# Optimization experiments

Measured on AMD Instinct MI355X. Metric: run time of the kernel, lower is better.

Reference implementation:

```python
import jax, jax.numpy as jnp
import numpy as np

B, N, E = 16, 2048, 1_048_576          # graphs, residues per graph, total edges
IN_C, DIM, OUT_C, ENC_H, N_ATOMS = 256, 128, 6, 100, 20
NT = B * N


def setup_inputs() -> dict:
    key = jax.random.key(0)
    ks = jax.random.split(key, 24)
    s = 0.02
    x_res = jax.random.normal(ks[0], (NT, IN_C), jnp.float32)
    coords = jax.random.normal(ks[1], (NT, 3), jnp.float32)
    batch = jnp.repeat(jnp.arange(B, dtype=jnp.int32), N)
    src = jax.random.randint(ks[2], (E,), 0, NT, dtype=jnp.int32)
    dst = (src // N) * N + jax.random.randint(ks[3], (E,), 0, N, dtype=jnp.int32)
    edge_index = jnp.stack([src, dst])  # intra-graph edges, global node ids
    return {
        'x_res': x_res, 'coords': coords,
        'edge_index': edge_index, 'batch': batch,
        'bn_gamma': jnp.ones((IN_C,), jnp.float32),
        'bn_beta': jnp.zeros((IN_C,), jnp.float32),
        'W1': s * jax.random.normal(ks[4], (IN_C, 2 * DIM), jnp.float32),
        'b1': jnp.zeros((2 * DIM,), jnp.float32),
        'W2': s * jax.random.normal(ks[5], (2 * DIM, DIM), jnp.float32),
        'b2': jnp.zeros((DIM,), jnp.float32),
        'W3': s * jax.random.normal(ks[6], (DIM, N_ATOMS), jnp.float32),
        'b3': jnp.zeros((N_ATOMS,), jnp.float32),
        'embed': s * jax.random.normal(ks[7], (N_ATOMS + 1, DIM), jnp.float32),
        'W_msg': s * jax.random.normal(ks[8], (DIM, DIM), jnp.float32),
        'b_msg': jnp.zeros((DIM,), jnp.float32),
        'w_coor': s * jax.random.normal(ks[9], (DIM, 3), jnp.float32),
        'A1': s * jax.random.normal(ks[10], (DIM, ENC_H), jnp.float32),
        'a1': jnp.zeros((ENC_H,), jnp.float32),
        'A2': s * jax.random.normal(ks[11], (ENC_H, OUT_C), jnp.float32),
        'a2': jnp.zeros((OUT_C,), jnp.float32),
        'dyt_alpha': jnp.float32(0.5),
        'dyt_w': jnp.ones((OUT_C,), jnp.float32),
        'dyt_b': jnp.zeros((OUT_C,), jnp.float32),
    }


def reference(x_res, coords, edge_index, batch,
              bn_gamma, bn_beta, W1, b1, W2, b2, W3, b3,
              embed, W_msg, b_msg, w_coor,
              A1, a1, A2, a2, dyt_alpha, dyt_w, dyt_b):
    gelu = lambda v: jax.nn.gelu(v, approximate=False)
    # BatchNorm1d (train-mode batch stats, biased var, eps=1e-5); dropout is identity in eval
    mu = x_res.mean(0)
    var = x_res.var(0)
    xn = (x_res - mu) / jnp.sqrt(var + 1e-5) * bn_gamma + bn_beta
    # input2atomids MLP -> argmax atom ids
    h1 = gelu(xn @ W1 + b1)
    h2 = gelu(h1 @ W2 + b2)
    logits = h2 @ W3 + b3
    ids = jnp.argmax(logits, axis=-1)          # [NT]
    ids_b = ids.reshape(B, N)                  # equal-sized graphs -> no padding needed
    coords_b = coords.reshape(B, N, 3)
    # vectorized edge-list -> dense per-graph adjacency scatter
    g = batch[edge_index[0]]                   # graph id per edge
    ls = edge_index[0] - g * N                 # local src index
    ld = edge_index[1] - g * N                 # local dst index
    same = batch[edge_index[1]] == g           # keep intra-graph edges only
    adj = jnp.zeros((B, N, N), jnp.bool_).at[g, ls, ld].max(same)
    # GotenNet stand-in: embed atom ids, one adjacency-masked aggregation layer
    emb_ids = jnp.where(ids_b < 0, N_ATOMS, ids_b)   # -1 pad -> pad embedding row
    h = embed[emb_ids]                          # [B,N,DIM]
    adjf = adj.astype(h.dtype)
    deg = jnp.maximum(adjf.sum(-1, keepdims=True), 1.0)
    m = jnp.einsum('bij,bjd->bid', adjf, h) / deg
    hout = gelu((h + m) @ W_msg + b_msg)        # invariant features [B,N,DIM]
    coors_out = coords_b + jnp.tanh(hout @ w_coor)
    # un-pad / flatten back to node list, then out_angles head
    z = hout.reshape(NT, DIM)
    t = gelu(z @ A1 + a1)
    t = gelu(t @ A2 + a2)
    t = jnp.tanh(dyt_alpha * t) * dyt_w + dyt_b  # DynamicTanh (channels_last)
    angles = jnp.tanh(t)                         # [NT, OUT_C]
    return angles, z, coors_out
```

## Files before the change

kernel.cpp:

```cpp
#include <hip/hip_runtime.h>
#include <hip/hip_bf16.h>
#include <math.h>

#define Bg 16
#define Nn 2048
#define Ee (1<<20)
#define NT (Bg*Nn)
#define INC 256
#define DIMd 128
#define OUTC 6
#define ENCH 100
#define NATOMS 20
#define BINCAP 3072

typedef __attribute__((ext_vector_type(8))) short bf16x8;
typedef __attribute__((ext_vector_type(4))) float f32x4;

__device__ __forceinline__ float gelu_f(float x){
    return 0.5f*x*(1.0f+erff(x*0.70710678118654752440f));
}
__device__ __forceinline__ unsigned short f2b(float f){
    __hip_bfloat16 h = __float2bfloat16(f);
    return *(unsigned short*)&h;
}
__device__ __forceinline__ float b2f(unsigned short u){
    unsigned v = ((unsigned)u)<<16;
    return __uint_as_float(v);
}
__device__ __forceinline__ void splitf(float v, unsigned short& hi, unsigned short& lo){
    unsigned short h = f2b(v);
    hi = h; lo = f2b(v - b2f(h));
}

__global__ __launch_bounds__(256) void prep0_k(const float* __restrict__ x,
    float* __restrict__ stats, const float* __restrict__ W1,
    const float* __restrict__ W2, const float* __restrict__ Wm,
    const float* __restrict__ A1, short* __restrict__ w1th, short* __restrict__ w1tl,
    short* __restrict__ w2th, short* __restrict__ w2tl,
    short* __restrict__ wmth, short* __restrict__ wmtl,
    short* __restrict__ a1th, short* __restrict__ a1tl)
{
    int bx = blockIdx.x, tid = threadIdx.x;
    if(bx < 256){
        int c = tid;
        int r0 = bx * 128;
        const float* p = x + (size_t)r0*INC + c;
        float s = 0.f, s2 = 0.f;
        #pragma unroll 8
        for(int r=0;r<128;r++){ float v = p[(size_t)r*INC]; s += v; s2 += v*v; }
        atomicAdd(&stats[c], s);
        atomicAdd(&stats[INC+c], s2);
    } else {
        int gid = (bx-256)*256 + tid;
        unsigned short hi, lo;
        for(int l=gid;l<65536;l+=16384){ int n=l>>8,k=l&255;
            splitf(W1[(size_t)k*256+n],hi,lo); w1th[l]=(short)hi; w1tl[l]=(short)lo; }
        for(int l=gid;l<32768;l+=16384){ int n=l>>8,k=l&255;
            splitf(W2[(size_t)k*128+n],hi,lo); w2th[l]=(short)hi; w2tl[l]=(short)lo; }
        for(int l=gid;l<16384;l+=16384){ int n=l>>7,k=l&127;
            splitf(Wm[(size_t)k*128+n],hi,lo); wmth[l]=(short)hi; wmtl[l]=(short)lo; }
        for(int l=gid;l<16384;l+=16384){ int n=l>>7,k=l&127;
            float v=(n<ENCH)? A1[(size_t)k*ENCH+n] : 0.f;
            splitf(v,hi,lo); a1th[l]=(short)hi; a1tl[l]=(short)lo; }
    }
}

__global__ __launch_bounds__(256) void gemm1_scat_k(const float* __restrict__ x,
    const float* __restrict__ stats, const float* __restrict__ gamma,
    const float* __restrict__ beta, const short* __restrict__ w1th,
    const short* __restrict__ w1tl, const float* __restrict__ b1,
    unsigned short* __restrict__ h1h, unsigned short* __restrict__ h1l,
    const int* __restrict__ ei, unsigned* __restrict__ ecnt,
    unsigned* __restrict__ earena)
{
    __shared__ float sc[256], sh[256];
    __shared__ short sAh[64*40], sAl[64*40];
    __shared__ short sBh[256*40], sBl[256*40];
    int tid = threadIdx.x;
    {
        float mu  = stats[tid]*(1.0f/NT);
        float var = stats[256+tid]*(1.0f/NT) - mu*mu;
        float s = gamma[tid]/sqrtf(var + 1e-5f);
        sc[tid] = s; sh[tid] = beta[tid] - mu*s;
    }
    int row0 = blockIdx.x*64;
    int lane = tid&63, w = tid>>6;
    int ln = lane&15, quad = lane>>4;
    int m0w = (w&1)*32, n0b = (w>>1)*128;
    f32x4 acc[2][8];
    #pragma unroll
    for(int i=0;i<2;i++)
        #pragma unroll
        for(int j=0;j<8;j++) acc[i][j] = (f32x4){0.f,0.f,0.f,0.f};

    float4 xa[2]; bf16x8 wb[8];
    #pragma unroll
    for(int i=0;i<2;i++){ int id=tid+i*256; int r=id>>3,kq=(id&7)*4;
        xa[i] = *(const float4*)&x[(size_t)(row0+r)*256 + kq]; }
    #pragma unroll
    for(int i=0;i<8;i++){ int id=tid+i*256; int plane=id>>10,cid=id&1023;
        int r=cid>>2,c=cid&3;
        wb[i] = *(const bf16x8*)((plane? w1tl:w1th) + (size_t)r*256 + c*8); }
    __syncthreads();
    for(int k0=0;k0<256;k0+=32){
        #pragma unroll
        for(int i=0;i<2;i++){
            int id = tid + i*256; int r = id>>3, kq = (id&7)*4;
            int k = k0+kq;
            float v0 = xa[i].x*sc[k]+sh[k],   v1 = xa[i].y*sc[k+1]+sh[k+1];
            float v2 = xa[i].z*sc[k+2]+sh[k+2], v3 = xa[i].w*sc[k+3]+sh[k+3];
            ushort4 hi, lo;
            splitf(v0,hi.x,lo.x); splitf(v1,hi.y,lo.y);
            splitf(v2,hi.z,lo.z); splitf(v3,hi.w,lo.w);
            *(ushort4*)&sAh[r*40+kq] = hi;
            *(ushort4*)&sAl[r*40+kq] = lo;
        }
        #pragma unroll
        for(int i=0;i<8;i++){
            int id = tid + i*256; int plane = id>>10, cid = id&1023;
            int r = cid>>2, c = cid&3;
            *(bf16x8*)((plane? sBl : sBh) + r*40 + c*8) = wb[i];
        }
        __syncthreads();
        if(k0 < 224){
            #pragma unroll
            for(int i=0;i<2;i++){ int id=tid+i*256; int r=id>>3,kq=(id&7)*4;
                xa[i] = *(const float4*)&x[(size_t)(row0+r)*256 + k0+32+kq]; }
            #pragma unroll
            for(int i=0;i<8;i++){ int id=tid+i*256; int plane=id>>10,cid=id&1023;
                int r=cid>>2,c=cid&3;
                wb[i] = *(const bf16x8*)((plane? w1tl:w1th) + (size_t)r*256 + k0+32 + c*8); }
        }
        bf16x8 ah[2], al[2];
        #pragma unroll
        for(int tm=0;tm<2;tm++){
            ah[tm] = *(const bf16x8*)&sAh[(m0w+tm*16+ln)*40 + quad*8];
            al[tm] = *(const bf16x8*)&sAl[(m0w+tm*16+ln)*40 + quad*8];
        }
        #pragma unroll
        for(int tn=0;tn<8;tn++){
            bf16x8 bh = *(const bf16x8*)&sBh[(n0b+tn*16+ln)*40 + quad*8];
            bf16x8 bl = *(const bf16x8*)&sBl[(n0b+tn*16+ln)*40 + quad*8];
            #pragma unroll
            for(int tm=0;tm<2;tm++){
                acc[tm][tn] = __builtin_amdgcn_mfma_f32_16x16x32_bf16(al[tm], bh, acc[tm][tn], 0,0,0);
                acc[tm][tn] = __builtin_amdgcn_mfma_f32_16x16x32_bf16(ah[tm], bl, acc[tm][tn], 0,0,0);
                acc[tm][tn] = __builtin_amdgcn_mfma_f32_16x16x32_bf16(ah[tm], bh, acc[tm][tn], 0,0,0);
            }
        }
        __syncthreads();
    }
    #pragma unroll
    for(int tn=0;tn<8;tn++){
        int col = n0b + tn*16 + ln;
        float bias = b1[col];
        #pragma unroll
        for(int tm=0;tm<2;tm++){
            int rowb = row0 + m0w + tm*16 + quad*4;
            #pragma unroll
            for(int r=0;r<4;r++){
                float hv = gelu_f(acc[tm][tn][r] + bias);
                unsigned short hi, lo;
                splitf(hv, hi, lo);
                h1h[(size_t)(rowb+r)*256 + col] = hi;
                h1l[(size_t)(rowb+r)*256 + col] = lo;
            }
        }
    }
    if(blockIdx.x < 128){
        __syncthreads();
        unsigned* lcnt  = (unsigned*)sAh;
        unsigned* gbase = ((unsigned*)sAh) + 512;
        for(int l=tid; l<512; l+=256) lcnt[l] = 0;
        __syncthreads();
        int ebase = blockIdx.x * 8192;
        #pragma unroll 8
        for(int i=0;i<32;i++){
            int e = ebase + i*256 + tid;
            int s = ei[e], d = ei[Ee+e];
            if((s>>11)==(d>>11)) atomicAdd(&lcnt[s>>6], 1u);
        }
        __syncthreads();
        for(int l=tid; l<512; l+=256){
            unsigned c = lcnt[l];
            gbase[l] = c ? atomicAdd(&ecnt[l], c) : 0u;
            lcnt[l] = 0;
        }
        __syncthreads();
        #pragma unroll 8
        for(int i=0;i<32;i++){
            int e = ebase + i*256 + tid;
            int s = ei[e], d = ei[Ee+e];
            if((s>>11)==(d>>11)){
                int bin = s>>6;
                unsigned r = atomicAdd(&lcnt[bin], 1u);
                unsigned pos = gbase[bin] + r;
                if(pos < BINCAP)
                    earena[(size_t)bin*BINCAP + pos] =
                        ((unsigned)(s&63)<<11) | (unsigned)(d&2047);
            }
        }
    }
}

__global__ __launch_bounds__(256) void gemm23_mfma(
    const unsigned short* __restrict__ h1h, const unsigned short* __restrict__ h1l,
    const short* __restrict__ w2th, const short* __restrict__ w2tl,
    const float* __restrict__ b2, const float* __restrict__ W3,
    const float* __restrict__ b3, int* __restrict__ ids)
{
    __shared__ short sAh[64*40], sAl[64*40];
    __shared__ short sBh[128*40], sBl[128*40];
    __shared__ float h2s[64*132];
    __shared__ float lgs[64*20];
    int tid = threadIdx.x;
    int row0 = blockIdx.x*64;
    int lane = tid&63, w = tid>>6;
    int ln = lane&15, quad = lane>>4;
    int m0w = (w&1)*32, n0w = (w>>1)*64;
    f32x4 acc[2][4];
    #pragma unroll
    for(int i=0;i<2;i++)
        #pragma unroll
        for(int j=0;j<4;j++) acc[i][j] = (f32x4){0.f,0.f,0.f,0.f};

    bf16x8 ha[2], wb[4];
    #pragma unroll
    for(int i=0;i<2;i++){ int id=tid+i*256; int plane=id>>8,cid=id&255;
        int r=cid>>2,c=cid&3;
        ha[i] = *(const bf16x8*)((const short*)(plane? h1l : h1h)
                                 + (size_t)(row0+r)*256 + c*8); }
    #pragma unroll
    for(int i=0;i<4;i++){ int id=tid+i*256; int plane=id>>9,cid=id&511;
        int r=cid>>2,c=cid&3;
        wb[i] = *(const bf16x8*)((plane? w2tl:w2th) + (size_t)r*256 + c*8); }
    for(int k0=0;k0<256;k0+=32){
        #pragma unroll
        for(int i=0;i<2;i++){
            int id = tid + i*256; int plane = id>>8, cid = id&255;
            int r = cid>>2, c = cid&3;
            *(bf16x8*)((plane? sAl : sAh) + r*40 + c*8) = ha[i];
        }
        #pragma unroll
        for(int i=0;i<4;i++){
            int id = tid + i*256; int plane = id>>9, cid = id&511;
            int r = cid>>2, c = cid&3;
            *(bf16x8*)((plane? sBl : sBh) + r*40 + c*8) = wb[i];
        }
        __syncthreads();
        if(k0 < 224){
            #pragma unroll
            for(int i=0;i<2;i++){ int id=tid+i*256; int plane=id>>8,cid=id&255;
                int r=cid>>2,c=cid&3;
                ha[i] = *(const bf16x8*)((const short*)(plane? h1l : h1h)
                                         + (size_t)(row0+r)*256 + k0+32 + c*8); }
            #pragma unroll
            for(int i=0;i<4;i++){ int id=tid+i*256; int plane=id>>9,cid=id&511;
                int r=cid>>2,c=cid&3;
                wb[i] = *(const bf16x8*)((plane? w2tl:w2th) + (size_t)r*256 + k0+32 + c*8); }
        }
        bf16x8 ah[2], al[2];
        #pragma unroll
        for(int tm=0;tm<2;tm++){
            ah[tm] = *(const bf16x8*)&sAh[(m0w+tm*16+ln)*40 + quad*8];
            al[tm] = *(const bf16x8*)&sAl[(m0w+tm*16+ln)*40 + quad*8];
        }
        #pragma unroll
        for(int tn=0;tn<4;tn++){
            bf16x8 bh = *(const bf16x8*)&sBh[(n0w+tn*16+ln)*40 + quad*8];
            bf16x8 bl = *(const bf16x8*)&sBl[(n0w+tn*16+ln)*40 + quad*8];
            #pragma unroll
            for(int tm=0;tm<2;tm++){
                acc[tm][tn] = __builtin_amdgcn_mfma_f32_16x16x32_bf16(al[tm], bh, acc[tm][tn], 0,0,0);
                acc[tm][tn] = __builtin_amdgcn_mfma_f32_16x16x32_bf16(ah[tm], bl, acc[tm][tn], 0,0,0);
                acc[tm][tn] = __builtin_amdgcn_mfma_f32_16x16x32_bf16(ah[tm], bh, acc[tm][tn], 0,0,0);
            }
        }
        __syncthreads();
    }
    #pragma unroll
    for(int tn=0;tn<4;tn++){
        int col = n0w + tn*16 + ln;
        float bias = b2[col];
        #pragma unroll
        for(int tm=0;tm<2;tm++){
            int rb = m0w + tm*16 + quad*4;
            #pragma unroll
            for(int r=0;r<4;r++)
                h2s[(rb+r)*132 + col] = gelu_f(acc[tm][tn][r] + bias);
        }
    }
    float* w3s = (float*)sBh;
    for(int l=tid;l<2560;l+=256) w3s[l] = W3[l];
    __syncthreads();
    int n = tid>>2, q = tid&3;
    float lg[5] = {};
    #pragma unroll 4
    for(int k=0;k<128;k++){
        float h = h2s[n*132+k];
        #pragma unroll
        for(int a=0;a<5;a++) lg[a] += h*w3s[k*20 + q*5 + a];
    }
    #pragma unroll
    for(int a=0;a<5;a++) lgs[n*20 + q*5 + a] = lg[a] + b3[q*5+a];
    __syncthreads();
    if(tid<64){
        float best = lgs[tid*20]; int bi = 0;
        #pragma unroll
        for(int a=1;a<20;a++){ float v2 = lgs[tid*20+a]; if(v2>best){best=v2;bi=a;} }
        ids[row0+tid] = bi;
    }
}

__global__ __launch_bounds__(256) void msgA_k(
    const int* __restrict__ ids, const unsigned* __restrict__ ecnt,
    const unsigned* __restrict__ earena, const float* __restrict__ embed,
    unsigned short* __restrict__ vbf)
{
    __shared__ unsigned lmask[64*64];
    __shared__ unsigned ind[NATOMS*64];
    __shared__ unsigned char sid[2048];
    __shared__ float emb[NATOMS*128];
    int tid = threadIdx.x;
    int bin = blockIdx.x;
    int row0 = bin*64;
    int g = bin>>5, tile = bin&31;
    int lane = tid&63, w = tid>>6;

    for(int l=tid;l<NATOMS*128;l+=256) emb[l] = embed[l];
    #pragma unroll
    for(int i=0;i<8;i++){ int j = tid + i*256; sid[j] = (unsigned char)ids[g*Nn + j]; }
    #pragma unroll
    for(int i=0;i<16;i++) lmask[tid + i*256] = 0;
    int nb = min((int)ecnt[bin], BINCAP);
    __syncthreads();

    for(int wp=w; wp<32; wp+=4){
        int a = sid[wp*64 + lane];
        #pragma unroll
        for(int atom=0; atom<NATOMS; atom++){
            unsigned long long bm = __ballot(a==atom);
            if(lane<2) ind[atom*64 + wp*2 + lane] = (unsigned)(bm >> (32*lane));
        }
    }
    for(int i=tid; i<nb; i+=256){
        unsigned wv = earena[(size_t)bin*BINCAP + i];
        int sl = wv>>11, dl = wv & 2047;
        atomicOr(&lmask[sl*64 + (dl>>5)], 1u<<(dl&31));
    }
    __syncthreads();

    int node = tid>>2, p = tid&3;
    unsigned mw[16];
    {
        const unsigned* mrow = &lmask[node*64 + p*16];
        *(uint4*)&mw[0]  = *(const uint4*)&mrow[0];
        *(uint4*)&mw[4]  = *(const uint4*)&mrow[4];
        *(uint4*)&mw[8]  = *(const uint4*)&mrow[8];
        *(uint4*)&mw[12] = *(const uint4*)&mrow[12];
    }
    int degi = 0;
    #pragma unroll
    for(int w2=0;w2<16;w2++) degi += __popc(mw[w2]);
    float cnt[NATOMS];
    #pragma unroll
    for(int a=0;a<NATOMS;a++){
        int c = 0;
        const unsigned* ia = &ind[a*64 + p*16];
        #pragma unroll
        for(int w2=0;w2<16;w2++) c += __popc(mw[w2] & ia[w2]);
        cnt[a] = (float)c;
    }
    #pragma unroll
    for(int a=0;a<NATOMS;a++){
        cnt[a] += __shfl_xor(cnt[a],1,64);
        cnt[a] += __shfl_xor(cnt[a],2,64);
    }
    float deg = (float)degi;
    deg += __shfl_xor(deg,1,64);
    deg += __shfl_xor(deg,2,64);

    {
        float inv = 1.0f / fmaxf(deg, 1.0f);
        int oid = sid[tile*64 + node];
        int d0 = p*32;
        float vv[32];
        #pragma unroll
        for(int d=0;d<32;d++) vv[d]=0.f;
        #pragma unroll
        for(int a=0;a<NATOMS;a++){
            float ca = cnt[a];
            const float* ea = &emb[a*128 + d0];
            #pragma unroll
            for(int d=0;d<32;d+=4){
                float4 e = *(const float4*)&ea[d];
                vv[d]+=ca*e.x; vv[d+1]+=ca*e.y; vv[d+2]+=ca*e.z; vv[d+3]+=ca*e.w;
            }
        }
        const float* eo = &emb[oid*128 + d0];
        unsigned short* dst = vbf + (size_t)(row0+node)*128 + d0;
        #pragma unroll
        for(int d=0;d<32;d+=4){
            float4 e = *(const float4*)&eo[d];
            ushort4 o;
            o.x = f2b(e.x + vv[d]*inv);
            o.y = f2b(e.y + vv[d+1]*inv);
            o.z = f2b(e.z + vv[d+2]*inv);
            o.w = f2b(e.w + vv[d+3]*inv);
            *(ushort4*)&dst[d] = o;
        }
    }
}

__global__ __launch_bounds__(256,4) void msgB_k(
    const unsigned short* __restrict__ vbf,
    const short* __restrict__ wmth, const short* __restrict__ wmtl,
    const float* __restrict__ b_msg, const float* __restrict__ w_coor,
    const short* __restrict__ a1th, const short* __restrict__ a1tl,
    const float* __restrict__ a1v, const float* __restrict__ A2,
    const float* __restrict__ a2v, const float* __restrict__ dalpha,
    const float* __restrict__ dw, const float* __restrict__ db,
    const float* __restrict__ coords, float* __restrict__ out_ang,
    float* __restrict__ out_z, float* __restrict__ out_co)
{
    __shared__ unsigned short houts[64*136];
    __shared__ float s_bm[128], s_wc[384], s_A2[624], s_a1[104];
    __shared__ float s_dyt[16], s_a2[8];
    int tid = threadIdx.x;
    int row0 = blockIdx.x*64;
    int lane = tid&63, w = tid>>6;
    int ln = lane&15, quad = lane>>4;
    int m0w = (w&1)*32, n0w = (w>>1)*64;

    if(tid<128) s_bm[tid] = b_msg[tid];
    if(tid<104) s_a1[tid] = (tid<ENCH) ? a1v[tid] : 0.f;
    for(int l=tid;l<384;l+=256) s_wc[l] = w_coor[l];
    for(int l=tid;l<624;l+=256) s_A2[l] = (l<600) ? A2[l] : 0.f;
    if(tid==0)  s_dyt[0] = dalpha[0];
    if(tid<6){ s_dyt[1+tid] = dw[tid]; s_dyt[8+tid] = db[tid]; }
    if(tid<8)  s_a2[tid] = (tid<6) ? a2v[tid] : 0.f;

    f32x4 acc[2][4];
    #pragma unroll
    for(int i=0;i<2;i++)
        #pragma unroll
        for(int j=0;j<4;j++) acc[i][j] = (f32x4){0.f,0.f,0.f,0.f};
    #pragma unroll
    for(int k0=0;k0<128;k0+=32){
        bf16x8 av[2];
        #pragma unroll
        for(int tm=0;tm<2;tm++)
            av[tm] = *(const bf16x8*)((const short*)vbf
                     + (size_t)(row0+m0w+tm*16+ln)*128 + k0 + quad*8);
        #pragma unroll
        for(int tn=0;tn<4;tn++){
            size_t bo = (size_t)(n0w+tn*16+ln)*128 + k0 + quad*8;
            bf16x8 bh = *(const bf16x8*)(wmth + bo);
            bf16x8 bl = *(const bf16x8*)(wmtl + bo);
            #pragma unroll
            for(int tm=0;tm<2;tm++){
                acc[tm][tn] = __builtin_amdgcn_mfma_f32_16x16x32_bf16(av[tm], bl, acc[tm][tn], 0,0,0);
                acc[tm][tn] = __builtin_amdgcn_mfma_f32_16x16x32_bf16(av[tm], bh, acc[tm][tn], 0,0,0);
            }
        }
    }
    __syncthreads();
    #pragma unroll
    for(int tn=0;tn<4;tn++){
        int col = n0w + tn*16 + ln;
        float bias = s_bm[col];
        #pragma unroll
        for(int tm=0;tm<2;tm++){
            int mb2 = m0w + tm*16 + quad*4;
            #pragma unroll
            for(int r=0;r<4;r++){
                float hv = gelu_f(acc[tm][tn][r] + bias);
                out_z[(size_t)(row0+mb2+r)*128 + col] = hv;
                houts[(mb2+r)*136 + col] = f2b(hv);
            }
        }
    }
    __syncthreads();

    int node = tid>>2, p = tid&3;
    {
        float d0=0.f, d1=0.f, d2=0.f;
        int kb = p*32;
        #pragma unroll
        for(int k=0;k<32;k+=4){
            ushort4 hv = *(const ushort4*)&houts[node*136 + kb + k];
            float h0=b2f(hv.x),h1=b2f(hv.y),h2=b2f(hv.z),h3=b2f(hv.w);
            const float* wc = &s_wc[(kb+k)*3];
            d0 += h0*wc[0]+h1*wc[3]+h2*wc[6]+h3*wc[9];
            d1 += h0*wc[1]+h1*wc[4]+h2*wc[7]+h3*wc[10];
            d2 += h0*wc[2]+h1*wc[5]+h2*wc[8]+h3*wc[11];
        }
        d0 += __shfl_xor(d0,1,64); d0 += __shfl_xor(d0,2,64);
        d1 += __shfl_xor(d1,1,64); d1 += __shfl_xor(d1,2,64);
        d2 += __shfl_xor(d2,1,64); d2 += __shfl_xor(d2,2,64);
        if(p==0){
            size_t o = (size_t)(row0+node)*3;
            out_co[o+0] = coords[o+0] + tanhf(d0);
            out_co[o+1] = coords[o+1] + tanhf(d1);
            out_co[o+2] = coords[o+2] + tanhf(d2);
        }
    }

    f32x4 acc2[2][4];
    #pragma unroll
    for(int i=0;i<2;i++)
        #pragma unroll
        for(int j=0;j<4;j++) acc2[i][j] = (f32x4){0.f,0.f,0.f,0.f};
    #pragma unroll
    for(int k0=0;k0<128;k0+=32){
        bf16x8 ah[2];
        #pragma unroll
        for(int tm=0;tm<2;tm++)
            ah[tm] = *(const bf16x8*)&houts[(m0w+tm*16+ln)*136 + k0 + quad*8];
        #pragma unroll
        for(int tn=0;tn<4;tn++){
            size_t bo = (size_t)(n0w+tn*16+ln)*128 + k0 + quad*8;
            bf16x8 bh = *(const bf16x8*)(a1th + bo);
            bf16x8 bl = *(const bf16x8*)(a1tl + bo);
            #pragma unroll
            for(int tm=0;tm<2;tm++){
                acc2[tm][tn] = __builtin_amdgcn_mfma_f32_16x16x32_bf16(ah[tm], bl, acc2[tm][tn], 0,0,0);
                acc2[tm][tn] = __builtin_amdgcn_mfma_f32_16x16x32_bf16(ah[tm], bh, acc2[tm][tn], 0,0,0);
            }
        }
    }
    __syncthreads();
    unsigned short* t1s = houts;
    #pragma unroll
    for(int tn=0;tn<4;tn++){
        int col = n0w + tn*16 + ln;
        if(col < 104){
            float bias = s_a1[col];
            #pragma unroll
            for(int tm=0;tm<2;tm++){
                int mb2 = m0w + tm*16 + quad*4;
                #pragma unroll
                for(int r=0;r<4;r++)
                    t1s[(mb2+r)*104 + col] = f2b(gelu_f(acc2[tm][tn][r] + bias));
            }
        }
    }
    __syncthreads();

    {
        int g0 = (p<2) ? p*7 : 14+(p-2)*6;
        int gcount = (p<2) ? 7 : 6;
        float s[6] = {0.f,0.f,0.f,0.f,0.f,0.f};
        for(int gg=0; gg<gcount; gg++){
            int kb = (g0+gg)*4;
            ushort4 tv = *(const ushort4*)&t1s[node*104 + kb];
            float u0=b2f(tv.x), u1=b2f(tv.y), u2=b2f(tv.z), u3=b2f(tv.w);
            #pragma unroll
            for(int j=0;j<6;j++)
                s[j] += u0*s_A2[kb*6+j] + u1*s_A2[(kb+1)*6+j]
                      + u2*s_A2[(kb+2)*6+j] + u3*s_A2[(kb+3)*6+j];
        }
        #pragma unroll
        for(int j=0;j<6;j++){ s[j]+=__shfl_xor(s[j],1,64); s[j]+=__shfl_xor(s[j],2,64); }
        if(p<2){
            size_t o = (size_t)(row0+node)*6 + p*3;
            #pragma unroll
            for(int jj=0;jj<3;jj++){
                int j = p*3+jj;
                float t2v = gelu_f(s[j] + s_a2[j]);
                float uu = tanhf(s_dyt[0]*t2v)*s_dyt[1+j] + s_dyt[8+j];
                out_ang[o+jj] = tanhf(uu);
            }
        }
    }
}

extern "C" void kernel_launch(void* const* d_in, const int* in_sizes, int n_in,
                              void* d_out, int out_size, void* d_ws, size_t ws_size,
                              hipStream_t stream) {
    const float* x      = (const float*)d_in[0];
    const float* coords = (const float*)d_in[1];
    const int*   ei     = (const int*)d_in[2];
    const float* gamma  = (const float*)d_in[4];
    const float* beta   = (const float*)d_in[5];
    const float* W1     = (const float*)d_in[6];
    const float* b1     = (const float*)d_in[7];
    const float* W2     = (const float*)d_in[8];
    const float* b2     = (const float*)d_in[9];
    const float* W3     = (const float*)d_in[10];
    const float* b3     = (const float*)d_in[11];
    const float* embed  = (const float*)d_in[12];
    const float* W_msg  = (const float*)d_in[13];
    const float* b_msg  = (const float*)d_in[14];
    const float* w_coor = (const float*)d_in[15];
    const float* A1     = (const float*)d_in[16];
    const float* a1v    = (const float*)d_in[17];
    const float* A2     = (const float*)d_in[18];
    const float* a2v    = (const float*)d_in[19];
    const float* dalpha = (const float*)d_in[20];
    const float* dw     = (const float*)d_in[21];
    const float* db     = (const float*)d_in[22];

    char* ws = (char*)d_ws;
    int*      ids   = (int*)ws;
    float*    stats = (float*)(ws + 131072);
    unsigned* ecnt  = (unsigned*)(ws + 131072 + 2048);
    short*    w1th  = (short*)(ws + 262144);
    short*    w1tl  = w1th + 65536;
    short*    w2th  = w1tl + 65536;
    short*    w2tl  = w2th + 32768;
    short*    wmth  = w2tl + 32768;
    short*    wmtl  = wmth + 16384;
    short*    a1th  = wmtl + 16384;
    short*    a1tl  = a1th + 16384;
    unsigned* earena = (unsigned*)(ws + (1<<20));
    unsigned short* h1h = (unsigned short*)(ws + (size_t)10*1048576);
    unsigned short* h1l = (unsigned short*)(ws + (size_t)27*1048576);
    unsigned short* vbf = h1h;

    float* out_ang = (float*)d_out;
    float* out_z   = out_ang + (size_t)NT*OUTC;
    float* out_co  = out_z   + (size_t)NT*DIMd;

    hipMemsetAsync(stats, 0, 4096, stream);
    prep0_k<<<320, 256, 0, stream>>>(x, stats, W1, W2, W_msg, A1,
        w1th, w1tl, w2th, w2tl, wmth, wmtl, a1th, a1tl);
    gemm1_scat_k<<<512, 256, 0, stream>>>(x, stats, gamma, beta, w1th, w1tl, b1,
        h1h, h1l, ei, ecnt, earena);
    gemm23_mfma<<<512, 256, 0, stream>>>(h1h, h1l, w2th, w2tl, b2, W3, b3, ids);
    msgA_k<<<512, 256, 0, stream>>>(ids, ecnt, earena, embed, vbf);
    msgB_k<<<512, 256, 0, stream>>>(vbf, wmth, wmtl, b_msg, w_coor,
        a1th, a1tl, a1v, A2, a2v, dalpha, dw, db, coords,
        out_ang, out_z, out_co);
}
```

Baseline: 271.3 us.

## Drop LDS staging in GEMM1/GEMM23, load MFMA fragments directly from global

Both MFMA GEMM kernels stop staging A and B tiles through shared memory with per-k-step barriers. Each wave now loads its bf16 fragments straight from global memory (L1/L2), and GEMM1 applies the BatchNorm and hi/lo split in registers. GEMM1 is also split across two column halves to give 1024 blocks, with launch bounds set for occupancy. This removes LDS traffic and barriers but adds redundant global/cache reads, and GEMM1 now reads x and normalises it twice (once per column half).

```diff
diff --git a/kernel.cpp b/kernel.cpp
--- a/kernel.cpp
+++ b/kernel.cpp
@@ -65,7 +65,7 @@
     }
 }
 
-__global__ __launch_bounds__(256) void gemm1_scat_k(const float* __restrict__ x,
+__global__ __launch_bounds__(256,4) void gemm1_scat_k(const float* __restrict__ x,
     const float* __restrict__ stats, const float* __restrict__ gamma,
     const float* __restrict__ beta, const short* __restrict__ w1th,
     const short* __restrict__ w1tl, const float* __restrict__ b1,
@@ -74,8 +74,7 @@
     unsigned* __restrict__ earena)
 {
     __shared__ float sc[256], sh[256];
-    __shared__ short sAh[64*40], sAl[64*40];
-    __shared__ short sBh[256*40], sBl[256*40];
+    __shared__ unsigned scat[1024];
     int tid = threadIdx.x;
     {
         float mu  = stats[tid]*(1.0f/NT);
@@ -83,64 +82,47 @@
         float s = gamma[tid]/sqrtf(var + 1e-5f);
         sc[tid] = s; sh[tid] = beta[tid] - mu*s;
     }
-    int row0 = blockIdx.x*64;
+    __syncthreads();
+    int bx = blockIdx.x;
+    int row0 = (bx & 511) * 64;
+    int colbase = (bx >> 9) * 128;
     int lane = tid&63, w = tid>>6;
     int ln = lane&15, quad = lane>>4;
-    int m0w = (w&1)*32, n0b = (w>>1)*128;
-    f32x4 acc[2][8];
+    int m0w = (w&1)*32, n0w = (w>>1)*64;
+    f32x4 acc[2][4];
     #pragma unroll
     for(int i=0;i<2;i++)
         #pragma unroll
-        for(int j=0;j<8;j++) acc[i][j] = (f32x4){0.f,0.f,0.f,0.f};
-
-    float4 xa[2]; bf16x8 wb[8];
-    #pragma unroll
-    for(int i=0;i<2;i++){ int id=tid+i*256; int r=id>>3,kq=(id&7)*4;
-        xa[i] = *(const float4*)&x[(size_t)(row0+r)*256 + kq]; }
-    #pragma unroll
-    for(int i=0;i<8;i++){ int id=tid+i*256; int plane=id>>10,cid=id&1023;
-        int r=cid>>2,c=cid&3;
-        wb[i] = *(const bf16x8*)((plane? w1tl:w1th) + (size_t)r*256 + c*8); }
-    __syncthreads();
+        for(int j=0;j<4;j++) acc[i][j] = (f32x4){0.f,0.f,0.f,0.f};
+
+    #pragma unroll 2
     for(int k0=0;k0<256;k0+=32){
-        #pragma unroll
-        for(int i=0;i<2;i++){
-            int id = tid + i*256; int r = id>>3, kq = (id&7)*4;
-            int k = k0+kq;
-            float v0 = xa[i].x*sc[k]+sh[k],   v1 = xa[i].y*sc[k+1]+sh[k+1];
-            float v2 = xa[i].z*sc[k+2]+sh[k+2], v3 = xa[i].w*sc[k+3]+sh[k+3];
-            ushort4 hi, lo;
-            splitf(v0,hi.x,lo.x); splitf(v1,hi.y,lo.y);
-            splitf(v2,hi.z,lo.z); splitf(v3,hi.w,lo.w);
-            *(ushort4*)&sAh[r*40+kq] = hi;
-            *(ushort4*)&sAl[r*40+kq] = lo;
-        }
-        #pragma unroll
-        for(int i=0;i<8;i++){
-            int id = tid + i*256; int plane = id>>10, cid = id&1023;
-            int r = cid>>2, c = cid&3;
-            *(bf16x8*)((plane? sBl : sBh) + r*40 + c*8) = wb[i];
-        }
-        __syncthreads();
-        if(k0 < 224){
-            #pragma unroll
-            for(int i=0;i<2;i++){ int id=tid+i*256; int r=id>>3,kq=(id&7)*4;
-                xa[i] = *(const float4*)&x[(size_t)(row0+r)*256 + k0+32+kq]; }
-            #pragma unroll
-            for(int i=0;i<8;i++){ int id=tid+i*256; int plane=id>>10,cid=id&1023;
-                int r=cid>>2,c=cid&3;
-                wb[i] = *(const bf16x8*)((plane? w1tl:w1th) + (size_t)r*256 + k0+32 + c*8); }
-        }
+        int kq = k0 + quad*8;
+        float4 sc0 = *(const float4*)&sc[kq];
+        float4 sc1 = *(const float4*)&sc[kq+4];
+        float4 sh0 = *(const float4*)&sh[kq];
+        float4 sh1 = *(const float4*)&sh[kq+4];
         bf16x8 ah[2], al[2];
         #pragma unroll
         for(int tm=0;tm<2;tm++){
-            ah[tm] = *(const bf16x8*)&sAh[(m0w+tm*16+ln)*40 + quad*8];
-            al[tm] = *(const bf16x8*)&sAl[(m0w+tm*16+ln)*40 + quad*8];
-        }
-        #pragma unroll
-        for(int tn=0;tn<8;tn++){
-            bf16x8 bh = *(const bf16x8*)&sBh[(n0b+tn*16+ln)*40 + quad*8];
-            bf16x8 bl = *(const bf16x8*)&sBl[(n0b+tn*16+ln)*40 + quad*8];
+            int row = row0 + m0w + tm*16 + ln;
+            float4 xa = *(const float4*)&x[(size_t)row*256 + kq];
+            float4 xb = *(const float4*)&x[(size_t)row*256 + kq + 4];
+            unsigned short hi, lo;
+            splitf(xa.x*sc0.x+sh0.x, hi, lo); ah[tm][0]=(short)hi; al[tm][0]=(short)lo;
+            splitf(xa.y*sc0.y+sh0.y, hi, lo); ah[tm][1]=(short)hi; al[tm][1]=(short)lo;
+            splitf(xa.z*sc0.z+sh0.z, hi, lo); ah[tm][2]=(short)hi; al[tm][2]=(short)lo;
+            splitf(xa.w*sc0.w+sh0.w, hi, lo); ah[tm][3]=(short)hi; al[tm][3]=(short)lo;
+            splitf(xb.x*sc1.x+sh1.x, hi, lo); ah[tm][4]=(short)hi; al[tm][4]=(short)lo;
+            splitf(xb.y*sc1.y+sh1.y, hi, lo); ah[tm][5]=(short)hi; al[tm][5]=(short)lo;
+            splitf(xb.z*sc1.z+sh1.z, hi, lo); ah[tm][6]=(short)hi; al[tm][6]=(short)lo;
+            splitf(xb.w*sc1.w+sh1.w, hi, lo); ah[tm][7]=(short)hi; al[tm][7]=(short)lo;
+        }
+        #pragma unroll
+        for(int tn=0;tn<4;tn++){
+            size_t bo = (size_t)(colbase + n0w + tn*16 + ln)*256 + kq;
+            bf16x8 bh = *(const bf16x8*)(w1th + bo);
+            bf16x8 bl = *(const bf16x8*)(w1tl + bo);
             #pragma unroll
             for(int tm=0;tm<2;tm++){
                 acc[tm][tn] = __builtin_amdgcn_mfma_f32_16x16x32_bf16(al[tm], bh, acc[tm][tn], 0,0,0);
@@ -148,11 +130,10 @@
                 acc[tm][tn] = __builtin_amdgcn_mfma_f32_16x16x32_bf16(ah[tm], bh, acc[tm][tn], 0,0,0);
             }
         }
-        __syncthreads();
-    }
-    #pragma unroll
-    for(int tn=0;tn<8;tn++){
-        int col = n0b + tn*16 + ln;
+    }
+    #pragma unroll
+    for(int tn=0;tn<4;tn++){
+        int col = colbase + n0w + tn*16 + ln;
         float bias = b1[col];
         #pragma unroll
         for(int tm=0;tm<2;tm++){
@@ -167,13 +148,12 @@
             }
         }
     }
-    if(blockIdx.x < 128){
-        __syncthreads();
-        unsigned* lcnt  = (unsigned*)sAh;
-        unsigned* gbase = ((unsigned*)sAh) + 512;
+    if(bx < 128){
+        unsigned* lcnt  = scat;
+        unsigned* gbase = scat + 512;
         for(int l=tid; l<512; l+=256) lcnt[l] = 0;
         __syncthreads();
-        int ebase = blockIdx.x * 8192;
+        int ebase = bx * 8192;
         #pragma unroll 8
         for(int i=0;i<32;i++){
             int e = ebase + i*256 + tid;
@@ -209,9 +189,8 @@
     const float* __restrict__ b2, const float* __restrict__ W3,
     const float* __restrict__ b3, int* __restrict__ ids)
 {
-    __shared__ short sAh[64*40], sAl[64*40];
-    __shared__ short sBh[128*40], sBl[128*40];
     __shared__ float h2s[64*132];
+    __shared__ float w3s[2560];
     __shared__ float lgs[64*20];
     int tid = threadIdx.x;
     int row0 = blockIdx.x*64;
@@ -224,51 +203,23 @@
         #pragma unroll
         for(int j=0;j<4;j++) acc[i][j] = (f32x4){0.f,0.f,0.f,0.f};
 
-    bf16x8 ha[2], wb[4];
-    #pragma unroll
-    for(int i=0;i<2;i++){ int id=tid+i*256; int plane=id>>8,cid=id&255;
-        int r=cid>>2,c=cid&3;
-        ha[i] = *(const bf16x8*)((const short*)(plane? h1l : h1h)
-                                 + (size_t)(row0+r)*256 + c*8); }
-    #pragma unroll
-    for(int i=0;i<4;i++){ int id=tid+i*256; int plane=id>>9,cid=id&511;
-        int r=cid>>2,c=cid&3;
-        wb[i] = *(const bf16x8*)((plane? w2tl:w2th) + (size_t)r*256 + c*8); }
+    for(int l=tid;l<2560;l+=256) w3s[l] = W3[l];
+
+    #pragma unroll 2
     for(int k0=0;k0<256;k0+=32){
-        #pragma unroll
-        for(int i=0;i<2;i++){
-            int id = tid + i*256; int plane = id>>8, cid = id&255;
-            int r = cid>>2, c = cid&3;
-            *(bf16x8*)((plane? sAl : sAh) + r*40 + c*8) = ha[i];
-        }
-        #pragma unroll
-        for(int i=0;i<4;i++){
-            int id = tid + i*256; int plane = id>>9, cid = id&511;
-            int r = cid>>2, c = cid&3;
-            *(bf16x8*)((plane? sBl : sBh) + r*40 + c*8) = wb[i];
-        }
-        __syncthreads();
-        if(k0 < 224){
-            #pragma unroll
-            for(int i=0;i<2;i++){ int id=tid+i*256; int plane=id>>8,cid=id&255;
-                int r=cid>>2,c=cid&3;
-                ha[i] = *(const bf16x8*)((const short*)(plane? h1l : h1h)
-                                         + (size_t)(row0+r)*256 + k0+32 + c*8); }
-            #pragma unroll
-            for(int i=0;i<4;i++){ int id=tid+i*256; int plane=id>>9,cid=id&511;
-                int r=cid>>2,c=cid&3;
-                wb[i] = *(const bf16x8*)((plane? w2tl:w2th) + (size_t)r*256 + k0+32 + c*8); }
-        }
+        int kq = k0 + quad*8;
         bf16x8 ah[2], al[2];
         #pragma unroll
         for(int tm=0;tm<2;tm++){
-            ah[tm] = *(const bf16x8*)&sAh[(m0w+tm*16+ln)*40 + quad*8];
-            al[tm] = *(const bf16x8*)&sAl[(m0w+tm*16+ln)*40 + quad*8];
+            size_t ao = (size_t)(row0 + m0w + tm*16 + ln)*256 + kq;
+            ah[tm] = *(const bf16x8*)((const short*)h1h + ao);
+            al[tm] = *(const bf16x8*)((const short*)h1l + ao);
         }
         #pragma unroll
         for(int tn=0;tn<4;tn++){
-            bf16x8 bh = *(const bf16x8*)&sBh[(n0w+tn*16+ln)*40 + quad*8];
-            bf16x8 bl = *(const bf16x8*)&sBl[(n0w+tn*16+ln)*40 + quad*8];
+            size_t bo = (size_t)(n0w + tn*16 + ln)*256 + kq;
+            bf16x8 bh = *(const bf16x8*)(w2th + bo);
+            bf16x8 bl = *(const bf16x8*)(w2tl + bo);
             #pragma unroll
             for(int tm=0;tm<2;tm++){
                 acc[tm][tn] = __builtin_amdgcn_mfma_f32_16x16x32_bf16(al[tm], bh, acc[tm][tn], 0,0,0);
@@ -276,7 +227,6 @@
                 acc[tm][tn] = __builtin_amdgcn_mfma_f32_16x16x32_bf16(ah[tm], bh, acc[tm][tn], 0,0,0);
             }
         }
-        __syncthreads();
     }
     #pragma unroll
     for(int tn=0;tn<4;tn++){
@@ -290,8 +240,6 @@
                 h2s[(rb+r)*132 + col] = gelu_f(acc[tm][tn][r] + bias);
         }
     }
-    float* w3s = (float*)sBh;
-    for(int l=tid;l<2560;l+=256) w3s[l] = W3[l];
     __syncthreads();
     int n = tid>>2, q = tid&3;
     float lg[5] = {};
@@ -625,7 +573,7 @@
     hipMemsetAsync(stats, 0, 4096, stream);
     prep0_k<<<320, 256, 0, stream>>>(x, stats, W1, W2, W_msg, A1,
         w1th, w1tl, w2th, w2tl, wmth, wmtl, a1th, a1tl);
-    gemm1_scat_k<<<512, 256, 0, stream>>>(x, stats, gamma, beta, w1th, w1tl, b1,
+    gemm1_scat_k<<<1024, 256, 0, stream>>>(x, stats, gamma, beta, w1th, w1tl, b1,
         h1h, h1l, ei, ecnt, earena);
     gemm23_mfma<<<512, 256, 0, stream>>>(h1h, h1l, w2th, w2tl, b2, W3, b3, ids);
     msgA_k<<<512, 256, 0, stream>>>(ids, ecnt, earena, embed, vbf);
```

After: 317.6 us. 17.1% more time.

## Split BN normalization into own kernel and move edge scatter into prep kernel

Applied to the files above, without the earlier changes.

Moves the edge-binning scatter from the tail of the GEMM1 kernel into extra blocks of the prep kernel, so it runs alongside the stats and weight-split work. Adds a separate kernel that applies BatchNorm and splits x into bf16 hi/lo planes. GEMM1 then reads those planes directly and writes its output in place over the same buffers. This takes the per-tile normalize/split work and the serialized scatter tail out of GEMM1, at the cost of an extra launch and an extra round trip of the normalized x through global memory.

```diff
diff --git a/kernel.cpp b/kernel.cpp
--- a/kernel.cpp
+++ b/kernel.cpp
@@ -38,8 +38,11 @@
     const float* __restrict__ A1, short* __restrict__ w1th, short* __restrict__ w1tl,
     short* __restrict__ w2th, short* __restrict__ w2tl,
     short* __restrict__ wmth, short* __restrict__ wmtl,
-    short* __restrict__ a1th, short* __restrict__ a1tl)
+    short* __restrict__ a1th, short* __restrict__ a1tl,
+    const int* __restrict__ ei, unsigned* __restrict__ ecnt,
+    unsigned* __restrict__ earena)
 {
+    __shared__ unsigned scat[1024];
     int bx = blockIdx.x, tid = threadIdx.x;
     if(bx < 256){
         int c = tid;
@@ -50,7 +53,7 @@
         for(int r=0;r<128;r++){ float v = p[(size_t)r*INC]; s += v; s2 += v*v; }
         atomicAdd(&stats[c], s);
         atomicAdd(&stats[INC+c], s2);
-    } else {
+    } else if(bx < 320){
         int gid = (bx-256)*256 + tid;
         unsigned short hi, lo;
         for(int l=gid;l<65536;l+=16384){ int n=l>>8,k=l&255;
@@ -62,118 +65,12 @@
         for(int l=gid;l<16384;l+=16384){ int n=l>>7,k=l&127;
             float v=(n<ENCH)? A1[(size_t)k*ENCH+n] : 0.f;
             splitf(v,hi,lo); a1th[l]=(short)hi; a1tl[l]=(short)lo; }
-    }
-}
-
-__global__ __launch_bounds__(256) void gemm1_scat_k(const float* __restrict__ x,
-    const float* __restrict__ stats, const float* __restrict__ gamma,
-    const float* __restrict__ beta, const short* __restrict__ w1th,
-    const short* __restrict__ w1tl, const float* __restrict__ b1,
-    unsigned short* __restrict__ h1h, unsigned short* __restrict__ h1l,
-    const int* __restrict__ ei, unsigned* __restrict__ ecnt,
-    unsigned* __restrict__ earena)
-{
-    __shared__ float sc[256], sh[256];
-    __shared__ short sAh[64*40], sAl[64*40];
-    __shared__ short sBh[256*40], sBl[256*40];
-    int tid = threadIdx.x;
-    {
-        float mu  = stats[tid]*(1.0f/NT);
-        float var = stats[256+tid]*(1.0f/NT) - mu*mu;
-        float s = gamma[tid]/sqrtf(var + 1e-5f);
-        sc[tid] = s; sh[tid] = beta[tid] - mu*s;
-    }
-    int row0 = blockIdx.x*64;
-    int lane = tid&63, w = tid>>6;
-    int ln = lane&15, quad = lane>>4;
-    int m0w = (w&1)*32, n0b = (w>>1)*128;
-    f32x4 acc[2][8];
-    #pragma unroll
-    for(int i=0;i<2;i++)
-        #pragma unroll
-        for(int j=0;j<8;j++) acc[i][j] = (f32x4){0.f,0.f,0.f,0.f};
-
-    float4 xa[2]; bf16x8 wb[8];
-    #pragma unroll
-    for(int i=0;i<2;i++){ int id=tid+i*256; int r=id>>3,kq=(id&7)*4;
-        xa[i] = *(const float4*)&x[(size_t)(row0+r)*256 + kq]; }
-    #pragma unroll
-    for(int i=0;i<8;i++){ int id=tid+i*256; int plane=id>>10,cid=id&1023;
-        int r=cid>>2,c=cid&3;
-        wb[i] = *(const bf16x8*)((plane? w1tl:w1th) + (size_t)r*256 + c*8); }
-    __syncthreads();
-    for(int k0=0;k0<256;k0+=32){
-        #pragma unroll
-        for(int i=0;i<2;i++){
-            int id = tid + i*256; int r = id>>3, kq = (id&7)*4;
-            int k = k0+kq;
-            float v0 = xa[i].x*sc[k]+sh[k],   v1 = xa[i].y*sc[k+1]+sh[k+1];
-            float v2 = xa[i].z*sc[k+2]+sh[k+2], v3 = xa[i].w*sc[k+3]+sh[k+3];
-            ushort4 hi, lo;
-            splitf(v0,hi.x,lo.x); splitf(v1,hi.y,lo.y);
-            splitf(v2,hi.z,lo.z); splitf(v3,hi.w,lo.w);
-            *(ushort4*)&sAh[r*40+kq] = hi;
-            *(ushort4*)&sAl[r*40+kq] = lo;
-        }
-        #pragma unroll
-        for(int i=0;i<8;i++){
-            int id = tid + i*256; int plane = id>>10, cid = id&1023;
-            int r = cid>>2, c = cid&3;
-            *(bf16x8*)((plane? sBl : sBh) + r*40 + c*8) = wb[i];
-        }
-        __syncthreads();
-        if(k0 < 224){
-            #pragma unroll
-            for(int i=0;i<2;i++){ int id=tid+i*256; int r=id>>3,kq=(id&7)*4;
-                xa[i] = *(const float4*)&x[(size_t)(row0+r)*256 + k0+32+kq]; }
-            #pragma unroll
-            for(int i=0;i<8;i++){ int id=tid+i*256; int plane=id>>10,cid=id&1023;
-                int r=cid>>2,c=cid&3;
-                wb[i] = *(const bf16x8*)((plane? w1tl:w1th) + (size_t)r*256 + k0+32 + c*8); }
-        }
-        bf16x8 ah[2], al[2];
-        #pragma unroll
-        for(int tm=0;tm<2;tm++){
-            ah[tm] = *(const bf16x8*)&sAh[(m0w+tm*16+ln)*40 + quad*8];
-            al[tm] = *(const bf16x8*)&sAl[(m0w+tm*16+ln)*40 + quad*8];
-        }
-        #pragma unroll
-        for(int tn=0;tn<8;tn++){
-            bf16x8 bh = *(const bf16x8*)&sBh[(n0b+tn*16+ln)*40 + quad*8];
-            bf16x8 bl = *(const bf16x8*)&sBl[(n0b+tn*16+ln)*40 + quad*8];
-            #pragma unroll
-            for(int tm=0;tm<2;tm++){
-                acc[tm][tn] = __builtin_amdgcn_mfma_f32_16x16x32_bf16(al[tm], bh, acc[tm][tn], 0,0,0);
-                acc[tm][tn] = __builtin_amdgcn_mfma_f32_16x16x32_bf16(ah[tm], bl, acc[tm][tn], 0,0,0);
-                acc[tm][tn] = __builtin_amdgcn_mfma_f32_16x16x32_bf16(ah[tm], bh, acc[tm][tn], 0,0,0);
-            }
-        }
-        __syncthreads();
-    }
-    #pragma unroll
-    for(int tn=0;tn<8;tn++){
-        int col = n0b + tn*16 + ln;
-        float bias = b1[col];
-        #pragma unroll
-        for(int tm=0;tm<2;tm++){
-            int rowb = row0 + m0w + tm*16 + quad*4;
-            #pragma unroll
-            for(int r=0;r<4;r++){
-                float hv = gelu_f(acc[tm][tn][r] + bias);
-                unsigned short hi, lo;
-                splitf(hv, hi, lo);
-                h1h[(size_t)(rowb+r)*256 + col] = hi;
-                h1l[(size_t)(rowb+r)*256 + col] = lo;
-            }
-        }
-    }
-    if(blockIdx.x < 128){
-        __syncthreads();
-        unsigned* lcnt  = (unsigned*)sAh;
-        unsigned* gbase = ((unsigned*)sAh) + 512;
+    } else {
+        unsigned* lcnt  = scat;
+        unsigned* gbase = scat + 512;
         for(int l=tid; l<512; l+=256) lcnt[l] = 0;
         __syncthreads();
-        int ebase = blockIdx.x * 8192;
+        int ebase = (bx-320) * 8192;
         #pragma unroll 8
         for(int i=0;i<32;i++){
             int e = ebase + i*256 + tid;
@@ -198,6 +95,118 @@
                 if(pos < BINCAP)
                     earena[(size_t)bin*BINCAP + pos] =
                         ((unsigned)(s&63)<<11) | (unsigned)(d&2047);
+            }
+        }
+    }
+}
+
+__global__ __launch_bounds__(256) void bnx_k(const float* __restrict__ x,
+    const float* __restrict__ stats, const float* __restrict__ gamma,
+    const float* __restrict__ beta,
+    unsigned short* __restrict__ xnh, unsigned short* __restrict__ xnl)
+{
+    __shared__ float sc[256], sh[256];
+    int tid = threadIdx.x;
+    {
+        float mu  = stats[tid]*(1.0f/NT);
+        float var = stats[256+tid]*(1.0f/NT) - mu*mu;
+        float s = gamma[tid]/sqrtf(var + 1e-5f);
+        sc[tid] = s; sh[tid] = beta[tid] - mu*s;
+    }
+    __syncthreads();
+    int gid = blockIdx.x*256 + tid;
+    int r = gid>>5, kq = (gid&31)*8;
+    size_t off = (size_t)r*256 + kq;
+    float4 a = *(const float4*)&x[off];
+    float4 b = *(const float4*)&x[off+4];
+    float va[8] = {a.x,a.y,a.z,a.w,b.x,b.y,b.z,b.w};
+    unsigned short hv[8], lv[8];
+    #pragma unroll
+    for(int i=0;i<8;i++)
+        splitf(va[i]*sc[kq+i]+sh[kq+i], hv[i], lv[i]);
+    *(ushort4*)&xnh[off]   = make_ushort4(hv[0],hv[1],hv[2],hv[3]);
+    *(ushort4*)&xnh[off+4] = make_ushort4(hv[4],hv[5],hv[6],hv[7]);
+    *(ushort4*)&xnl[off]   = make_ushort4(lv[0],lv[1],lv[2],lv[3]);
+    *(ushort4*)&xnl[off+4] = make_ushort4(lv[4],lv[5],lv[6],lv[7]);
+}
+
+__global__ __launch_bounds__(256) void gemm1_k(
+    unsigned short* xh, unsigned short* xl,
+    const short* __restrict__ w1th, const short* __restrict__ w1tl,
+    const float* __restrict__ b1)
+{
+    __shared__ short sAh[64*40], sAl[64*40];
+    __shared__ short sBh[256*40], sBl[256*40];
+    int tid = threadIdx.x;
+    int row0 = blockIdx.x*64;
+    int lane = tid&63, w = tid>>6;
+    int ln = lane&15, quad = lane>>4;
+    int m0w = (w&1)*32, n0b = (w>>1)*128;
+    f32x4 acc[2][8];
+    #pragma unroll
+    for(int i=0;i<2;i++)
+        #pragma unroll
+        for(int j=0;j<8;j++) acc[i][j] = (f32x4){0.f,0.f,0.f,0.f};
+
+    int ar = tid>>2, ac = tid&3;
+    bf16x8 xah, xal; bf16x8 wb[8];
+    xah = *(const bf16x8*)(xh + (size_t)(row0+ar)*256 + ac*8);
+    xal = *(const bf16x8*)(xl + (size_t)(row0+ar)*256 + ac*8);
+    #pragma unroll
+    for(int i=0;i<8;i++){ int id=tid+i*256; int plane=id>>10,cid=id&1023;
+        int r=cid>>2,c=cid&3;
+        wb[i] = *(const bf16x8*)((plane? w1tl:w1th) + (size_t)r*256 + c*8); }
+    for(int k0=0;k0<256;k0+=32){
+        *(bf16x8*)&sAh[ar*40 + ac*8] = xah;
+        *(bf16x8*)&sAl[ar*40 + ac*8] = xal;
+        #pragma unroll
+        for(int i=0;i<8;i++){
+            int id = tid + i*256; int plane = id>>10, cid = id&1023;
+            int r = cid>>2, c = cid&3;
+            *(bf16x8*)((plane? sBl : sBh) + r*40 + c*8) = wb[i];
+        }
+        __syncthreads();
+        if(k0 < 224){
+            xah = *(const bf16x8*)(xh + (size_t)(row0+ar)*256 + k0+32 + ac*8);
+            xal = *(const bf16x8*)(xl + (size_t)(row0+ar)*256 + k0+32 + ac*8);
+            #pragma unroll
+            for(int i=0;i<8;i++){ int id=tid+i*256; int plane=id>>10,cid=id&1023;
+                int r=cid>>2,c=cid&3;
+                wb[i] = *(const bf16x8*)((plane? w1tl:w1th) + (size_t)r*256 + k0+32 + c*8); }
+        }
+        bf16x8 ah[2], al[2];
+        #pragma unroll
+        for(int tm=0;tm<2;tm++){
+            ah[tm] = *(const bf16x8*)&sAh[(m0w+tm*16+ln)*40 + quad*8];
+            al[tm] = *(const bf16x8*)&sAl[(m0w+tm*16+ln)*40 + quad*8];
+        }
+        #pragma unroll
+        for(int tn=0;tn<8;tn++){
+            bf16x8 bh = *(const bf16x8*)&sBh[(n0b+tn*16+ln)*40 + quad*8];
+            bf16x8 bl = *(const bf16x8*)&sBl[(n0b+tn*16+ln)*40 + quad*8];
+            #pragma unroll
+            for(int tm=0;tm<2;tm++){
+                acc[tm][tn] = __builtin_amdgcn_mfma_f32_16x16x32_bf16(al[tm], bh, acc[tm][tn], 0,0,0);
+                acc[tm][tn] = __builtin_amdgcn_mfma_f32_16x16x32_bf16(ah[tm], bl, acc[tm][tn], 0,0,0);
+                acc[tm][tn] = __builtin_amdgcn_mfma_f32_16x16x32_bf16(ah[tm], bh, acc[tm][tn], 0,0,0);
+            }
+        }
+        __syncthreads();
+    }
+    #pragma unroll
+    for(int tn=0;tn<8;tn++){
+        int col = n0b + tn*16 + ln;
+        float bias = b1[col];
+        #pragma unroll
+        for(int tm=0;tm<2;tm++){
+            int rowb = row0 + m0w + tm*16 + quad*4;
+            #pragma unroll
+            for(int r=0;r<4;r++){
+                float hv = gelu_f(acc[tm][tn][r] + bias);
+                unsigned short hi, lo;
+                splitf(hv, hi, lo);
+                xh[(size_t)(rowb+r)*256 + col] = hi;
+                xl[(size_t)(rowb+r)*256 + col] = lo;
             }
         }
     }
@@ -623,10 +632,10 @@
     float* out_co  = out_z   + (size_t)NT*DIMd;
 
     hipMemsetAsync(stats, 0, 4096, stream);
-    prep0_k<<<320, 256, 0, stream>>>(x, stats, W1, W2, W_msg, A1,
-        w1th, w1tl, w2th, w2tl, wmth, wmtl, a1th, a1tl);
-    gemm1_scat_k<<<512, 256, 0, stream>>>(x, stats, gamma, beta, w1th, w1tl, b1,
-        h1h, h1l, ei, ecnt, earena);
+    prep0_k<<<448, 256, 0, stream>>>(x, stats, W1, W2, W_msg, A1,
+        w1th, w1tl, w2th, w2tl, wmth, wmtl, a1th, a1tl, ei, ecnt, earena);
+    bnx_k<<<4096, 256, 0, stream>>>(x, stats, gamma, beta, h1h, h1l);
+    gemm1_k<<<512, 256, 0, stream>>>(h1h, h1l, w1th, w1tl, b1);
     gemm23_mfma<<<512, 256, 0, stream>>>(h1h, h1l, w2th, w2tl, b2, W3, b3, ids);
     msgA_k<<<512, 256, 0, stream>>>(ids, ecnt, earena, embed, vbf);
     msgB_k<<<512, 256, 0, stream>>>(vbf, wmth, wmtl, b_msg, w_coor,
```

New measurement: 279.2 us. 1.03x slower.
